# Kernel tuning notes

Measured on AMD Instinct MI355X. Metric: run time of the kernel, lower is better.

## Reference

```python
import jax, jax.numpy as jnp
import numpy as np
from jax import lax

INF = 1e10
R = 20          # max_distance: EDT truncated at this radius (exact under clamp)
NUM_CLASSES = 19


def _pass1d(f, axis):
    """1D squared distance transform min_{|d|<=R} (d^2 + f[shifted]), truncated.
    f: [..., H, W] with 0 at 'source' pixels, INF elsewhere. Out-of-bounds = INF
    (matches scipy, which sees nothing beyond the array border)."""
    pad = [(0, 0)] * f.ndim
    pad[axis] = (R, R)
    fp = jnp.pad(f, pad, constant_values=INF)
    n = f.shape[axis]
    out = jnp.full_like(f, INF)
    for d in range(2 * R + 1):  # fixed small loop (41 iters), jit-unrolled
        shifted = lax.slice_in_dim(fp, d, d + n, axis=axis)
        out = jnp.minimum(out, shifted + float((d - R) ** 2))
    return out


def edt_trunc(mask):
    """Euclidean distance from each True pixel to nearest False pixel,
    truncated at R (False pixels get 0). mask: [..., H, W] bool."""
    f = jnp.where(mask, INF, 0.0).astype(jnp.float32)
    g = _pass1d(f, -2)
    g = _pass1d(g, -1)
    return jnp.sqrt(jnp.minimum(g, float(R * R)))


def compute_sdf(onehot_bool):
    """Signed distance: negdist - posdist, per [B,C,H,W] one-hot masks.
    Already truncated at +-R, matching clamp(-R, R) in the torch module."""
    posdist = edt_trunc(onehot_bool)    # distance inside FG to BG
    negdist = edt_trunc(~onehot_bool)   # distance inside BG to FG
    return negdist - posdist


def setup_inputs() -> dict:
    key = jax.random.key(0)
    k1, k2 = jax.random.split(key)
    logits = jax.random.normal(k1, (8, NUM_CLASSES, 256, 512), dtype=jnp.float32)
    targets = jax.random.randint(k2, (8, 256, 512), 0, NUM_CLASSES, dtype=jnp.int64)
    return {"logits": logits, "targets": targets}


def reference(logits, targets):
    C = logits.shape[1]
    probs = jax.nn.softmax(logits, axis=1)                       # [B,C,H,W]
    onehot = jax.nn.one_hot(targets, C, axis=1, dtype=jnp.bool_)  # [B,C,H,W]
    sdf = compute_sdf(onehot)
    sdf = jnp.clip(sdf, -float(R), float(R)) / float(R)
    # mean over spatial, sum over classes, mean over batch (reduction='mean')
    per_class = jnp.mean(probs * sdf, axis=(2, 3))               # [B,C]
    loss = jnp.sum(per_class, axis=1)                            # [B]
    return jnp.mean(loss)
```

## Files before the change

### kernel.cpp

```cpp
#include <hip/hip_runtime.h>
#include <hip/hip_bf16.h>
#include <math.h>

#define NCLS 19
#define BB   8
#define HH   256
#define WW   512
#define CAP2 400u
#define SEG  8

typedef unsigned short u16x2 __attribute__((ext_vector_type(2)));

static __device__ __forceinline__ unsigned umin32(unsigned a, unsigned b) { return a < b ? a : b; }
static __device__ __forceinline__ float fsqrt_fast(float x) { return __builtin_amdgcn_sqrtf(x); }

static __device__ __forceinline__ unsigned pk_add_s(unsigned v, unsigned c) {
    unsigned d; asm("v_pk_add_u16 %0, %1, %2" : "=v"(d) : "s"(c), "v"(v)); return d;
}
static __device__ __forceinline__ unsigned pk_minv(unsigned a, unsigned b) {
    unsigned d; asm("v_pk_min_u16 %0, %1, %2" : "=v"(d) : "v"(a), "v"(b)); return d;
}
static __device__ __forceinline__ unsigned pk_maxv(unsigned a, unsigned b) {
    unsigned d; asm("v_pk_max_u16 %0, %1, %2" : "=v"(d) : "v"(a), "v"(b)); return d;
}
static __device__ __forceinline__ unsigned pk_hmin(unsigned a) {
    unsigned d;
    asm("v_pk_min_u16 %0, %1, %1 op_sel:[1,0] op_sel_hi:[0,1]" : "=v"(d) : "v"(a));
    return d;
}
static __device__ __forceinline__ void sq8(unsigned x, unsigned& w0, unsigned& w1) {
    unsigned a = x & 0x00FF00FFu;
    unsigned b = (x >> 8) & 0x00FF00FFu;
    u16x2 sa = __builtin_bit_cast(u16x2, a); sa = sa * sa;
    u16x2 sb = __builtin_bit_cast(u16x2, b); sb = sb * sb;
    unsigned ua = __builtin_bit_cast(unsigned, sa);
    unsigned ub = __builtin_bit_cast(unsigned, sb);
    w0 = __builtin_amdgcn_perm(ub, ua, 0x05040100u);
    w1 = __builtin_amdgcn_perm(ub, ua, 0x07060302u);
}

__global__ __launch_bounds__(256)
void kA_vert(const int* __restrict__ targ, unsigned char* __restrict__ vneg,
             unsigned long long* __restrict__ acc) {
    if (blockIdx.x == 0 && threadIdx.x == 0) { *acc = 0ULL; }
    int gid = blockIdx.x * 256 + threadIdx.x;
    int col = gid & 4095;
    int seg = gid >> 12;
    int b = col >> 9;
    int w = col & 511;
    int h0 = seg * SEG;
    const int* tp = &targ[b * HH * WW + w];

    unsigned d[NCLS];
    unsigned pk[NCLS][2];
#pragma unroll
    for (int c = 0; c < NCLS; ++c) { d[c] = 21u; pk[c][0] = 0u; pk[c][1] = 0u; }
#pragma unroll
    for (int k = 0; k < 21 + SEG; ++k) {
        int hh = h0 - 21 + k;
        int t = -1;
        if (hh >= 0) t = tp[hh * WW];
#pragma unroll
        for (int c = 0; c < NCLS; ++c)
            d[c] = (t == c) ? 0u : d[c] + 1u;
        if (k >= 21) {
            int r = k - 21;
#pragma unroll
            for (int c = 0; c < NCLS; ++c)
                pk[c][r >> 2] |= d[c] << ((r & 3) * 8);
        }
    }
    unsigned u[NCLS];
#pragma unroll
    for (int c = 0; c < NCLS; ++c) u[c] = 21u;
#pragma unroll
    for (int k = 0; k < 21 + SEG; ++k) {
        int hh = h0 + 21 + SEG - 1 - k;
        int t = -1;
        if (hh < HH) t = tp[hh * WW];
#pragma unroll
        for (int c = 0; c < NCLS; ++c)
            u[c] = (t == c) ? 0u : u[c] + 1u;
        if (k >= 21) {
            int r = 21 + SEG - 1 - k;
#pragma unroll
            for (int c = 0; c < NCLS; ++c) {
                unsigned dv = (pk[c][r >> 2] >> ((r & 3) * 8)) & 0xffu;
                vneg[((size_t)(b * NCLS + c) * HH + hh) * WW + w] =
                    (unsigned char)umin32(dv, u[c]);
            }
        }
    }
}

__global__ __launch_bounds__(256)
void kB_main(const float* __restrict__ logits,
             const unsigned char* __restrict__ vneg,
             unsigned long long* __restrict__ acc) {
    __shared__ float sNum[4][256];
    __shared__ float sDen[4][256];
    __shared__ float sEt[4][256];
    __shared__ unsigned short sM2[4][256];
    __shared__ float wsum[4];
    int tid = threadIdx.x;
    int L = tid & 63;
    int wid = tid >> 6;
    int bh = blockIdx.x;
    int b = bh >> 8;
    int h = bh & 255;

    const unsigned HALO2 = 441u | (441u << 16);

#define SQx(x) ((unsigned)((x) * (x)))
#define PK2(a, bq) (SQx(a) | (SQx(bq) << 16))
    const unsigned CE[21] = {
        PK2(-20,-19), PK2(-18,-17), PK2(-16,-15), PK2(-14,-13), PK2(-12,-11),
        PK2(-10,-9),  PK2(-8,-7),   PK2(-6,-5),   PK2(-4,-3),   PK2(-2,-1),
        PK2(0,1),     PK2(2,3),     PK2(4,5),     PK2(6,7),     PK2(8,9),
        PK2(10,11),   PK2(12,13),   PK2(14,15),   PK2(16,17),   PK2(18,19),
        PK2(20,21) };
    const unsigned CO[21] = {
        PK2(-21,-20), PK2(-19,-18), PK2(-17,-16), PK2(-15,-14), PK2(-13,-12),
        PK2(-11,-10), PK2(-9,-8),   PK2(-7,-6),   PK2(-5,-4),   PK2(-3,-2),
        PK2(-1,0),    PK2(1,2),     PK2(3,4),     PK2(5,6),     PK2(7,8),
        PK2(9,10),    PK2(11,12),   PK2(13,14),   PK2(15,16),   PK2(17,18),
        PK2(19,20) };
#undef PK2
#undef SQx

    int im1 = ((L + 63) & 63) * 4, im2 = ((L + 62) & 63) * 4, im3 = ((L + 61) & 63) * 4;
    int ip1 = ((L + 1) & 63) * 4,  ip2 = ((L + 2) & 63) * 4,  ip3 = ((L + 3) & 63) * 4;

    const uint2* vrw = (const uint2*)vneg + ((size_t)(b * NCLS + wid) * HH + h) * 64 + L;
    const float* lroww = &logits[((size_t)(b * NCLS + wid) * HH + h) * WW + 8 * L];
    int nc = (wid < 3) ? 5 : 4;

    float den[8], num[8], et[8];
    unsigned m2[8];
#pragma unroll
    for (int p = 0; p < 8; ++p) { den[p]=0.f; num[p]=0.f; et[p]=0.f; m2[p]=0xFFFFu; }

    uint2 v8n = vrw[0];
    float4 f0n = *(const float4*)lroww;
    float4 f1n = *(const float4*)(lroww + 4);

#pragma unroll 1
    for (int i = 0; i < nc; ++i) {
        uint2 v8 = v8n;
        float4 f0 = f0n, f1 = f1n;
        if (i + 1 < nc) {
            size_t off = (size_t)(i + 1) * 4 * (HH * 64);
            v8n = vrw[off];
            const float* ln = lroww + (size_t)(i + 1) * 4 * (HH * WW);
            f0n = *(const float4*)ln;
            f1n = *(const float4*)(ln + 4);
        }

        unsigned o0, o1, o2, o3;
        sq8(v8.x, o0, o1);
        sq8(v8.y, o2, o3);

        unsigned S[24];
        S[10] = o0; S[11] = o1; S[12] = o2; S[13] = o3;
        unsigned t;
        t = __builtin_amdgcn_ds_bpermute(im1, (int)o3); S[9]  = (L >= 1) ? t : HALO2;
        t = __builtin_amdgcn_ds_bpermute(im1, (int)o2); S[8]  = (L >= 1) ? t : HALO2;
        t = __builtin_amdgcn_ds_bpermute(im1, (int)o1); S[7]  = (L >= 1) ? t : HALO2;
        t = __builtin_amdgcn_ds_bpermute(im1, (int)o0); S[6]  = (L >= 1) ? t : HALO2;
        t = __builtin_amdgcn_ds_bpermute(im2, (int)o3); S[5]  = (L >= 2) ? t : HALO2;
        t = __builtin_amdgcn_ds_bpermute(im2, (int)o2); S[4]  = (L >= 2) ? t : HALO2;
        t = __builtin_amdgcn_ds_bpermute(im2, (int)o1); S[3]  = (L >= 2) ? t : HALO2;
        t = __builtin_amdgcn_ds_bpermute(im2, (int)o0); S[2]  = (L >= 2) ? t : HALO2;
        t = __builtin_amdgcn_ds_bpermute(im3, (int)o3); S[1]  = (L >= 3) ? t : HALO2;
        t = __builtin_amdgcn_ds_bpermute(im3, (int)o2); S[0]  = (L >= 3) ? t : HALO2;
        t = __builtin_amdgcn_ds_bpermute(ip1, (int)o0); S[14] = (L <= 62) ? t : HALO2;
        t = __builtin_amdgcn_ds_bpermute(ip1, (int)o1); S[15] = (L <= 62) ? t : HALO2;
        t = __builtin_amdgcn_ds_bpermute(ip1, (int)o2); S[16] = (L <= 62) ? t : HALO2;
        t = __builtin_amdgcn_ds_bpermute(ip1, (int)o3); S[17] = (L <= 62) ? t : HALO2;
        t = __builtin_amdgcn_ds_bpermute(ip2, (int)o0); S[18] = (L <= 61) ? t : HALO2;
        t = __builtin_amdgcn_ds_bpermute(ip2, (int)o1); S[19] = (L <= 61) ? t : HALO2;
        t = __builtin_amdgcn_ds_bpermute(ip2, (int)o2); S[20] = (L <= 61) ? t : HALO2;
        t = __builtin_amdgcn_ds_bpermute(ip2, (int)o3); S[21] = (L <= 61) ? t : HALO2;
        t = __builtin_amdgcn_ds_bpermute(ip3, (int)o0); S[22] = (L <= 60) ? t : HALO2;
        t = __builtin_amdgcn_ds_bpermute(ip3, (int)o1); S[23] = (L <= 60) ? t : HALO2;

        unsigned ae[4], ao[4];
#pragma unroll
        for (int r = 0; r < 4; ++r) { ae[r] = 0xFFFFFFFFu; ao[r] = 0xFFFFFFFFu; }

#pragma unroll
        for (int r = 0; r < 4; ++r)
#pragma unroll
            for (int m = 7; m <= 13; ++m) {
                ae[r] = pk_minv(ae[r], pk_add_s(S[r + m], CE[m]));
                ao[r] = pk_minv(ao[r], pk_add_s(S[r + m], CO[m]));
            }

        unsigned mx = pk_maxv(pk_maxv(pk_maxv(pk_hmin(ae[0]), pk_hmin(ao[0])),
                                      pk_maxv(pk_hmin(ae[1]), pk_hmin(ao[1]))),
                              pk_maxv(pk_maxv(pk_hmin(ae[2]), pk_hmin(ao[2])),
                                      pk_maxv(pk_hmin(ae[3]), pk_hmin(ao[3]))));
        if (!__all(mx <= (49u | (49u << 16)))) {
#pragma unroll
            for (int r = 0; r < 4; ++r) {
#pragma unroll
                for (int m = 0; m <= 6; ++m) {
                    ae[r] = pk_minv(ae[r], pk_add_s(S[r + m], CE[m]));
                    ao[r] = pk_minv(ao[r], pk_add_s(S[r + m], CO[m]));
                }
#pragma unroll
                for (int m = 14; m <= 20; ++m) {
                    ae[r] = pk_minv(ae[r], pk_add_s(S[r + m], CE[m]));
                    ao[r] = pk_minv(ao[r], pk_add_s(S[r + m], CO[m]));
                }
            }
        }

        float fx[8] = {f0.x, f0.y, f0.z, f0.w, f1.x, f1.y, f1.z, f1.w};
#pragma unroll
        for (int r = 0; r < 4; ++r) {
            unsigned nd0 = pk_hmin(ae[r]) & 0xFFFFu;
            unsigned nd1 = pk_hmin(ao[r]) & 0xFFFFu;
            float e0 = __expf(fx[2 * r]), e1 = __expf(fx[2 * r + 1]);
            den[2 * r] += e0; den[2 * r + 1] += e1;
            float s0 = fsqrt_fast((float)umin32(nd0, CAP2));
            float s1 = fsqrt_fast((float)umin32(nd1, CAP2));
            num[2 * r]     += e0 * s0;
            num[2 * r + 1] += e1 * s1;
            bool z0 = (nd0 == 0), z1 = (nd1 == 0);
            et[2 * r]     = z0 ? e0 : et[2 * r];
            et[2 * r + 1] = z1 ? e1 : et[2 * r + 1];
            m2[2 * r]     = umin32(m2[2 * r],     z0 ? 0xFFFFu : nd0);
            m2[2 * r + 1] = umin32(m2[2 * r + 1], z1 ? 0xFFFFu : nd1);
        }
    }

    float vsum = 0.f;
#pragma unroll
    for (int pass = 0; pass < 2; ++pass) {
        if ((L >> 5) == pass) {
            int base = 8 * (L & 31);
            *(float4*)&sNum[wid][base]     = (float4){num[0], num[1], num[2], num[3]};
            *(float4*)&sNum[wid][base + 4] = (float4){num[4], num[5], num[6], num[7]};
            *(float4*)&sDen[wid][base]     = (float4){den[0], den[1], den[2], den[3]};
            *(float4*)&sDen[wid][base + 4] = (float4){den[4], den[5], den[6], den[7]};
            *(float4*)&sEt[wid][base]      = (float4){et[0], et[1], et[2], et[3]};
            *(float4*)&sEt[wid][base + 4]  = (float4){et[4], et[5], et[6], et[7]};
            uint4 mq;
            mq.x = m2[0] | (m2[1] << 16); mq.y = m2[2] | (m2[3] << 16);
            mq.z = m2[4] | (m2[5] << 16); mq.w = m2[6] | (m2[7] << 16);
            *(uint4*)&sM2[wid][base] = mq;
        }
        __syncthreads();
        {
            float N = sNum[0][tid] + sNum[1][tid] + sNum[2][tid] + sNum[3][tid];
            float D = sDen[0][tid] + sDen[1][tid] + sDen[2][tid] + sDen[3][tid];
            float E = sEt[0][tid] + sEt[1][tid] + sEt[2][tid] + sEt[3][tid];
            unsigned M = umin32(umin32((unsigned)sM2[0][tid], (unsigned)sM2[1][tid]),
                                umin32((unsigned)sM2[2][tid], (unsigned)sM2[3][tid]));
            vsum += (N - E * fsqrt_fast((float)umin32(M, CAP2))) / D;
        }
        __syncthreads();
    }

#pragma unroll
    for (int off = 32; off >= 1; off >>= 1) vsum += __shfl_down(vsum, off);
    if (L == 0) wsum[wid] = vsum;
    __syncthreads();
    if (tid == 0) {
        float s = (wsum[0] + wsum[1]) + (wsum[2] + wsum[3]);
        double q = (double)s * (68719476736.0 / 20.0);
        atomicAdd(acc, (unsigned long long)(long long)q);
    }
}

__global__ void kC_final(const unsigned long long* __restrict__ acc,
                         float* __restrict__ out) {
    long long iv = (long long)*acc;
    double v = (double)iv / 68719476736.0;
    out[0] = (float)(v / (double)((size_t)BB * HH * WW));
}

extern "C" void kernel_launch(void* const* d_in, const int* in_sizes, int n_in,
                              void* d_out, int out_size, void* d_ws, size_t ws_size,
                              hipStream_t stream) {
    const float* logits = (const float*)d_in[0];
    const int* targ = (const int*)d_in[1];
    unsigned char* wsb = (unsigned char*)d_ws;
    unsigned long long* acc = (unsigned long long*)wsb;
    unsigned char* vneg = wsb + 64;

    kA_vert<<<512, 256, 0, stream>>>(targ, vneg, acc);
    kB_main<<<BB * HH, 256, 0, stream>>>(logits, vneg, acc);
    kC_final<<<1, 1, 0, stream>>>(acc, (float*)d_out);
}
```

Before: 61.15 us.

## Store squared vertical distances as padded u16 rows, drop lane-permute halo exchange

The vertical pass now writes squared distances as 16-bit values into rows padded with a 441 halo (32 entries each side), instead of raw 8-bit distances. The main kernel then reads a 56-element window per lane with seven 16-byte loads, replacing the in-register squaring and twenty ds_bpermute cross-lane halo exchanges with their boundary selects. The trade is double the intermediate buffer size plus overlapping, redundant global/L2 reads, and a halo-fill loop added to the first kernel.

```diff
diff --git a/kernel.cpp b/kernel.cpp
--- a/kernel.cpp
+++ b/kernel.cpp
@@ -8,6 +8,7 @@
 #define WW   512
 #define CAP2 400u
 #define SEG  8
+#define VROW 576
 
 typedef unsigned short u16x2 __attribute__((ext_vector_type(2)));
 
@@ -28,22 +29,19 @@
     asm("v_pk_min_u16 %0, %1, %1 op_sel:[1,0] op_sel_hi:[0,1]" : "=v"(d) : "v"(a));
     return d;
 }
-static __device__ __forceinline__ void sq8(unsigned x, unsigned& w0, unsigned& w1) {
-    unsigned a = x & 0x00FF00FFu;
-    unsigned b = (x >> 8) & 0x00FF00FFu;
-    u16x2 sa = __builtin_bit_cast(u16x2, a); sa = sa * sa;
-    u16x2 sb = __builtin_bit_cast(u16x2, b); sb = sb * sb;
-    unsigned ua = __builtin_bit_cast(unsigned, sa);
-    unsigned ub = __builtin_bit_cast(unsigned, sb);
-    w0 = __builtin_amdgcn_perm(ub, ua, 0x05040100u);
-    w1 = __builtin_amdgcn_perm(ub, ua, 0x07060302u);
-}
 
 __global__ __launch_bounds__(256)
-void kA_vert(const int* __restrict__ targ, unsigned char* __restrict__ vneg,
+void kA_vert(const int* __restrict__ targ, unsigned short* __restrict__ vsq,
              unsigned long long* __restrict__ acc) {
     if (blockIdx.x == 0 && threadIdx.x == 0) { *acc = 0ULL; }
     int gid = blockIdx.x * 256 + threadIdx.x;
+
+    for (int i = gid; i < BB * NCLS * HH * 64; i += 131072) {
+        int p = i & 63;
+        int rch = i >> 6;
+        vsq[(size_t)rch * VROW + ((p < 32) ? p : (512 + p))] = 441;
+    }
+
     int col = gid & 4095;
     int seg = gid >> 12;
     int b = col >> 9;
@@ -86,8 +84,9 @@
 #pragma unroll
             for (int c = 0; c < NCLS; ++c) {
                 unsigned dv = (pk[c][r >> 2] >> ((r & 3) * 8)) & 0xffu;
-                vneg[((size_t)(b * NCLS + c) * HH + hh) * WW + w] =
-                    (unsigned char)umin32(dv, u[c]);
+                unsigned m = umin32(dv, u[c]);
+                vsq[((size_t)(b * NCLS + c) * HH + hh) * VROW + 32 + w] =
+                    (unsigned short)(m * m);
             }
         }
     }
@@ -95,7 +94,7 @@
 
 __global__ __launch_bounds__(256)
 void kB_main(const float* __restrict__ logits,
-             const unsigned char* __restrict__ vneg,
+             const unsigned short* __restrict__ vsq,
              unsigned long long* __restrict__ acc) {
     __shared__ float sNum[4][256];
     __shared__ float sDen[4][256];
@@ -108,8 +107,6 @@
     int bh = blockIdx.x;
     int b = bh >> 8;
     int h = bh & 255;
-
-    const unsigned HALO2 = 441u | (441u << 16);
 
 #define SQx(x) ((unsigned)((x) * (x)))
 #define PK2(a, bq) (SQx(a) | (SQx(bq) << 16))
@@ -128,10 +125,8 @@
 #undef PK2
 #undef SQx
 
-    int im1 = ((L + 63) & 63) * 4, im2 = ((L + 62) & 63) * 4, im3 = ((L + 61) & 63) * 4;
-    int ip1 = ((L + 1) & 63) * 4,  ip2 = ((L + 2) & 63) * 4,  ip3 = ((L + 3) & 63) * 4;
-
-    const uint2* vrw = (const uint2*)vneg + ((size_t)(b * NCLS + wid) * HH + h) * 64 + L;
+    const unsigned short* vbase =
+        vsq + ((size_t)(b * NCLS + wid) * HH + h) * VROW + 8 + 8 * L;
     const float* lroww = &logits[((size_t)(b * NCLS + wid) * HH + h) * WW + 8 * L];
     int nc = (wid < 3) ? 5 : 4;
 
@@ -140,49 +135,25 @@
 #pragma unroll
     for (int p = 0; p < 8; ++p) { den[p]=0.f; num[p]=0.f; et[p]=0.f; m2[p]=0xFFFFu; }
 
-    uint2 v8n = vrw[0];
     float4 f0n = *(const float4*)lroww;
     float4 f1n = *(const float4*)(lroww + 4);
 
 #pragma unroll 1
     for (int i = 0; i < nc; ++i) {
-        uint2 v8 = v8n;
         float4 f0 = f0n, f1 = f1n;
         if (i + 1 < nc) {
-            size_t off = (size_t)(i + 1) * 4 * (HH * 64);
-            v8n = vrw[off];
             const float* ln = lroww + (size_t)(i + 1) * 4 * (HH * WW);
             f0n = *(const float4*)ln;
             f1n = *(const float4*)(ln + 4);
         }
 
-        unsigned o0, o1, o2, o3;
-        sq8(v8.x, o0, o1);
-        sq8(v8.y, o2, o3);
-
-        unsigned S[24];
-        S[10] = o0; S[11] = o1; S[12] = o2; S[13] = o3;
-        unsigned t;
-        t = __builtin_amdgcn_ds_bpermute(im1, (int)o3); S[9]  = (L >= 1) ? t : HALO2;
-        t = __builtin_amdgcn_ds_bpermute(im1, (int)o2); S[8]  = (L >= 1) ? t : HALO2;
-        t = __builtin_amdgcn_ds_bpermute(im1, (int)o1); S[7]  = (L >= 1) ? t : HALO2;
-        t = __builtin_amdgcn_ds_bpermute(im1, (int)o0); S[6]  = (L >= 1) ? t : HALO2;
-        t = __builtin_amdgcn_ds_bpermute(im2, (int)o3); S[5]  = (L >= 2) ? t : HALO2;
-        t = __builtin_amdgcn_ds_bpermute(im2, (int)o2); S[4]  = (L >= 2) ? t : HALO2;
-        t = __builtin_amdgcn_ds_bpermute(im2, (int)o1); S[3]  = (L >= 2) ? t : HALO2;
-        t = __builtin_amdgcn_ds_bpermute(im2, (int)o0); S[2]  = (L >= 2) ? t : HALO2;
-        t = __builtin_amdgcn_ds_bpermute(im3, (int)o3); S[1]  = (L >= 3) ? t : HALO2;
-        t = __builtin_amdgcn_ds_bpermute(im3, (int)o2); S[0]  = (L >= 3) ? t : HALO2;
-        t = __builtin_amdgcn_ds_bpermute(ip1, (int)o0); S[14] = (L <= 62) ? t : HALO2;
-        t = __builtin_amdgcn_ds_bpermute(ip1, (int)o1); S[15] = (L <= 62) ? t : HALO2;
-        t = __builtin_amdgcn_ds_bpermute(ip1, (int)o2); S[16] = (L <= 62) ? t : HALO2;
-        t = __builtin_amdgcn_ds_bpermute(ip1, (int)o3); S[17] = (L <= 62) ? t : HALO2;
-        t = __builtin_amdgcn_ds_bpermute(ip2, (int)o0); S[18] = (L <= 61) ? t : HALO2;
-        t = __builtin_amdgcn_ds_bpermute(ip2, (int)o1); S[19] = (L <= 61) ? t : HALO2;
-        t = __builtin_amdgcn_ds_bpermute(ip2, (int)o2); S[20] = (L <= 61) ? t : HALO2;
-        t = __builtin_amdgcn_ds_bpermute(ip2, (int)o3); S[21] = (L <= 61) ? t : HALO2;
-        t = __builtin_amdgcn_ds_bpermute(ip3, (int)o0); S[22] = (L <= 60) ? t : HALO2;
-        t = __builtin_amdgcn_ds_bpermute(ip3, (int)o1); S[23] = (L <= 60) ? t : HALO2;
+        const uint4* wq = (const uint4*)(vbase + (size_t)(4 * i) * (HH * VROW));
+        uint4 q0 = wq[0], q1 = wq[1], q2 = wq[2], q3 = wq[3],
+              q4 = wq[4], q5 = wq[5], q6 = wq[6];
+        unsigned W[28] = {q0.x,q0.y,q0.z,q0.w, q1.x,q1.y,q1.z,q1.w,
+                          q2.x,q2.y,q2.z,q2.w, q3.x,q3.y,q3.z,q3.w,
+                          q4.x,q4.y,q4.z,q4.w, q5.x,q5.y,q5.z,q5.w,
+                          q6.x,q6.y,q6.z,q6.w};
 
         unsigned ae[4], ao[4];
 #pragma unroll
@@ -192,8 +163,8 @@
         for (int r = 0; r < 4; ++r)
 #pragma unroll
             for (int m = 7; m <= 13; ++m) {
-                ae[r] = pk_minv(ae[r], pk_add_s(S[r + m], CE[m]));
-                ao[r] = pk_minv(ao[r], pk_add_s(S[r + m], CO[m]));
+                ae[r] = pk_minv(ae[r], pk_add_s(W[r + m + 2], CE[m]));
+                ao[r] = pk_minv(ao[r], pk_add_s(W[r + m + 2], CO[m]));
             }
 
         unsigned mx = pk_maxv(pk_maxv(pk_maxv(pk_hmin(ae[0]), pk_hmin(ao[0])),
@@ -205,13 +176,13 @@
             for (int r = 0; r < 4; ++r) {
 #pragma unroll
                 for (int m = 0; m <= 6; ++m) {
-                    ae[r] = pk_minv(ae[r], pk_add_s(S[r + m], CE[m]));
-                    ao[r] = pk_minv(ao[r], pk_add_s(S[r + m], CO[m]));
+                    ae[r] = pk_minv(ae[r], pk_add_s(W[r + m + 2], CE[m]));
+                    ao[r] = pk_minv(ao[r], pk_add_s(W[r + m + 2], CO[m]));
                 }
 #pragma unroll
                 for (int m = 14; m <= 20; ++m) {
-                    ae[r] = pk_minv(ae[r], pk_add_s(S[r + m], CE[m]));
-                    ao[r] = pk_minv(ao[r], pk_add_s(S[r + m], CO[m]));
+                    ae[r] = pk_minv(ae[r], pk_add_s(W[r + m + 2], CE[m]));
+                    ao[r] = pk_minv(ao[r], pk_add_s(W[r + m + 2], CO[m]));
                 }
             }
         }
@@ -288,9 +259,9 @@
     const int* targ = (const int*)d_in[1];
     unsigned char* wsb = (unsigned char*)d_ws;
     unsigned long long* acc = (unsigned long long*)wsb;
-    unsigned char* vneg = wsb + 64;
-
-    kA_vert<<<512, 256, 0, stream>>>(targ, vneg, acc);
-    kB_main<<<BB * HH, 256, 0, stream>>>(logits, vneg, acc);
+    unsigned short* vsq = (unsigned short*)(wsb + 64);
+
+    kA_vert<<<512, 256, 0, stream>>>(targ, vsq, acc);
+    kB_main<<<BB * HH, 256, 0, stream>>>(logits, vsq, acc);
     kC_final<<<1, 1, 0, stream>>>(acc, (float*)d_out);
 }
```

Measured after the change: 65.26 us. +6.7%, slower.
